# Performance work log

Hardware: AMD Instinct MI355X
Metric: run time of the kernel (lower is better)

The kernel has to match this reference:

```python
import jax, jax.numpy as jnp
import numpy as np

RADIUS = 5
KS = 2 * RADIUS + 1  # 11
SIGMA_X2 = 4.0 ** 2  # 16
SIGMA_I2 = 10.0 ** 2  # 100


def _patches(x):
    """x: [N,1,H,W] -> [N, H*W, KS, KS] zero-padded sliding windows (torch Unfold semantics)."""
    N, _, H, W = x.shape
    p = jax.lax.conv_general_dilated_patches(
        x, (KS, KS), (1, 1), [(RADIUS, RADIUS), (RADIUS, RADIUS)]
    )  # [N, KS*KS, H, W], channel dim ordered (kh, kw)
    return p.reshape(N, KS, KS, H * W).transpose(0, 3, 1, 2)


def _distance_map(dtype):
    d = (jnp.arange(KS, dtype=dtype) - RADIUS) ** 2
    return jnp.exp(-(d[:, None] + d[None, :]) / SIGMA_X2)  # [KS, KS]


def setup_inputs() -> dict:
    key = jax.random.key(0)
    k1, k2 = jax.random.split(key)
    images = jax.random.uniform(k1, (8, 1, 224, 224), dtype=jnp.float32)
    labels = jax.random.uniform(k2, (8, 4, 224, 224), dtype=jnp.float32)
    return {"images": images, "labels": labels}


def reference(images, labels):
    B, _, H, W = images.shape
    K = labels.shape[1]
    HW = H * W

    img = images * 255.0
    regions = _patches(img)                                   # [B,HW,KS,KS]
    mask = _patches(jnp.ones((1, 1, H, W), img.dtype))        # [1,HW,KS,KS], 0 on padding
    dist_map = _distance_map(img.dtype)                       # [KS,KS]

    i_f = img.reshape(B, HW)[:, :, None, None]                # center pixel intensity
    weights = dist_map * jnp.exp(-(regions - i_f) ** 2 / SIGMA_I2) * mask  # [B,HW,KS,KS]

    # class-prob patches for all classes at once
    P = _patches(labels.reshape(B * K, 1, H, W)).reshape(B, K, HW, KS, KS)

    num = jnp.einsum('bnij,bknij->bkn', weights, P)           # sum_j w_ij * p_j
    den = weights.sum(axis=(2, 3))                            # [B,HW], sum_j w_ij
    p_f = labels.reshape(B, K, HW)

    ratio = jnp.einsum('bkn,bkn->bk', p_f, num) / jnp.einsum('bkn,bn->bk', p_f, den)
    # per-class L1Loss(ratio, 0) = mean over batch of |ratio|; summed over classes
    ratio_sum = jnp.abs(ratio).mean(axis=0).sum()
    return K - ratio_sum
```

## Files before the change

kernel.cpp:

```cpp
#include <hip/hip_runtime.h>
#include <hip/hip_bf16.h>

typedef float f2 __attribute__((ext_vector_type(2)));
typedef float f4 __attribute__((ext_vector_type(4)));

constexpr int Hh = 224, Ww = 224, Bb = 8, Kc = 4, RAD = 5;

constexpr int TX = 32;
constexpr int TILEH = 16;
constexpr int SW = TX + 2 * RAD;
constexpr int SH = TILEH + 2 * RAD;
constexpr int SSTR = SW + 1;
constexpr int GXD = Ww / TX;
constexpr int GYD = Hh / TILEH;
constexpr int PB = GXD * GYD;

constexpr float LOG2E = 1.44269504f;
constexpr float KI = -0.01f * LOG2E;
constexpr float DSC = -0.0625f * LOG2E;
constexpr float D2[12] = {25.f,16.f,9.f,4.f,1.f,0.f,1.f,4.f,9.f,16.f,25.f,0.f};

static __device__ inline f4 splat4(float x) { return (f4){x, x, x, x}; }

__global__ __launch_bounds__(256, 3) void ncut_main(const float* __restrict__ images,
                                                    const float* __restrict__ labels,
                                                    float* __restrict__ acc) {
    __shared__ float simg[SH * SSTR];
    __shared__ f4    slab[SH * SSTR];
    __shared__ float red[4][8];

    const int b   = blockIdx.z;
    const int x0  = blockIdx.x * TX;
    const int y0  = blockIdx.y * TILEH;
    const int tid = threadIdx.x;

    const float* imgb = images + (size_t)b * (Hh * Ww);
    const float* labb = labels + (size_t)b * (Kc * Hh * Ww);

    for (int idx = tid; idx < SH * SSTR; idx += 256) {
        const int lx = idx % SSTR, ly = idx / SSTR;
        const int gx = x0 - RAD + lx, gy = y0 - RAD + ly;
        float iv = 1e19f;
        f4 lv = (f4){0.f, 0.f, 0.f, 0.f};
        if (lx < SW && gx >= 0 && gx < Ww && gy >= 0 && gy < Hh) {
            const int g = gy * Ww + gx;
            iv = imgb[g] * 255.0f;
            lv = (f4){labb[g], labb[Hh * Ww + g], labb[2 * Hh * Ww + g], labb[3 * Hh * Ww + g]};
        }
        simg[idx] = iv;
        slab[idx] = lv;
    }
    __syncthreads();

    const int tx = tid & 31;
    const int ty = tid >> 5;
    const int r0 = 2 * ty;

    const float c0 = simg[(r0 + RAD) * SSTR + tx + RAD];
    const float c1 = simg[(r0 + RAD + 1) * SSTR + tx + RAD];

    f4 num0 = splat4(0.f), num1 = splat4(0.f);
    f2 den0 = (f2){0.f, 0.f}, den1 = (f2){0.f, 0.f};

#pragma unroll
    for (int dr = 0; dr < 12; ++dr) {
        const int rowoff = (r0 + dr) * SSTR + tx;
#pragma unroll
        for (int i = 0; i < 6; ++i) {
            const f2 v  = (f2){simg[rowoff + 2 * i], simg[rowoff + 2 * i + 1]};
            const f4 p0 = slab[rowoff + 2 * i];
            const f4 p1 = slab[rowoff + 2 * i + 1];
            if (dr < 11) {
                const f2 base = (f2){(D2[2 * i] + D2[dr]) * DSC,
                                     (D2[2 * i + 1] + D2[dr]) * DSC};
                const f2 d = v - c0;
                const f2 a = __builtin_elementwise_fma(d * KI, d, base);
                const float e0 = __builtin_amdgcn_exp2f(a.x);
                const float e1 = __builtin_amdgcn_exp2f(a.y);
                den0 += (f2){e0, e1};
                num0 = __builtin_elementwise_fma(splat4(e0), p0, num0);
                num0 = __builtin_elementwise_fma(splat4(e1), p1, num0);
            }
            if (dr >= 1) {
                const f2 base = (f2){(D2[2 * i] + D2[dr - 1]) * DSC,
                                     (D2[2 * i + 1] + D2[dr - 1]) * DSC};
                const f2 d = v - c1;
                const f2 a = __builtin_elementwise_fma(d * KI, d, base);
                const float e0 = __builtin_amdgcn_exp2f(a.x);
                const float e1 = __builtin_amdgcn_exp2f(a.y);
                den1 += (f2){e0, e1};
                num1 = __builtin_elementwise_fma(splat4(e0), p0, num1);
                num1 = __builtin_elementwise_fma(splat4(e1), p1, num1);
            }
        }
    }

    const f4 pc0 = slab[(r0 + RAD) * SSTR + tx + RAD];
    const f4 pc1 = slab[(r0 + RAD + 1) * SSTR + tx + RAD];
    const float dn0 = den0.x + den0.y;
    const float dn1 = den1.x + den1.y;

    const f4 numv = pc0 * num0 + pc1 * num1;
    const f4 denv = pc0 * dn0 + pc1 * dn1;

    float vals[8] = {numv.x, numv.y, numv.z, numv.w, denv.x, denv.y, denv.z, denv.w};

#pragma unroll
    for (int i = 0; i < 8; ++i) {
        float v = vals[i];
#pragma unroll
        for (int off = 32; off > 0; off >>= 1) v += __shfl_down(v, off, 64);
        vals[i] = v;
    }

    const int wave = tid >> 6, lane = tid & 63;
    if (lane == 0) {
#pragma unroll
        for (int i = 0; i < 8; ++i) red[wave][i] = vals[i];
    }
    __syncthreads();

    if (tid < 8) {
        const int gid = blockIdx.x + GXD * blockIdx.y + GXD * GYD * blockIdx.z;
        acc[gid * 8 + tid] = red[0][tid] + red[1][tid] + red[2][tid] + red[3][tid];
    }
}

__global__ void ncut_final(const float* __restrict__ acc, float* __restrict__ out) {
    const int t = threadIdx.x;
    const int k = t & 3, b = (t >> 2) & 7, part = t >> 5;
    float s = 0.f;
    for (int j = 0; j < PB; ++j) s += acc[(b * PB + j) * 8 + k + 4 * part];
    const float den = __shfl(s, (t + 32) & 63, 64);
    float r = (t < 32) ? fabsf(s / den) : 0.f;
#pragma unroll
    for (int off = 32; off > 0; off >>= 1) r += __shfl_down(r, off, 64);
    if (t == 0) out[0] = (float)Kc - r * (1.0f / (float)Bb);
}

extern "C" void kernel_launch(void* const* d_in, const int* in_sizes, int n_in,
                              void* d_out, int out_size, void* d_ws, size_t ws_size,
                              hipStream_t stream) {
    const float* images = (const float*)d_in[0];
    const float* labels = (const float*)d_in[1];
    float* out = (float*)d_out;
    float* acc = (float*)d_ws;

    dim3 grid(GXD, GYD, Bb);
    ncut_main<<<grid, 256, 0, stream>>>(images, labels, acc);
    ncut_final<<<1, 64, 0, stream>>>(acc, out);
}
```

Measured before the change: 83.95 us.

## Compute four output rows per thread with 128-thread blocks and separable distance weights

Each thread now accumulates four vertically adjacent output pixels instead of two, so every shared-memory image and label load in a column window is reused across more centers. Blocks shrink to 128 threads. The spatial Gaussian is factored into an x term folded into the exponent and a per-row y weight that is multiplied after the exp. The row loop is no longer unrolled, and each weight costs an extra multiply. The loop also does some wasted work on out-of-band rows where the y weight is zero. Fewer threads per block and more registers per thread may reduce occupancy.

```diff
diff --git a/kernel.cpp b/kernel.cpp
--- a/kernel.cpp
+++ b/kernel.cpp
@@ -7,6 +7,7 @@
 constexpr int Hh = 224, Ww = 224, Bb = 8, Kc = 4, RAD = 5;
 
 constexpr int TX = 32;
+constexpr int T  = 4;
 constexpr int TILEH = 16;
 constexpr int SW = TX + 2 * RAD;
 constexpr int SH = TILEH + 2 * RAD;
@@ -16,18 +17,17 @@
 constexpr int PB = GXD * GYD;
 
 constexpr float LOG2E = 1.44269504f;
-constexpr float KI = -0.01f * LOG2E;
+constexpr float KI  = -0.01f * LOG2E;
 constexpr float DSC = -0.0625f * LOG2E;
-constexpr float D2[12] = {25.f,16.f,9.f,4.f,1.f,0.f,1.f,4.f,9.f,16.f,25.f,0.f};
 
 static __device__ inline f4 splat4(float x) { return (f4){x, x, x, x}; }
 
-__global__ __launch_bounds__(256, 3) void ncut_main(const float* __restrict__ images,
-                                                    const float* __restrict__ labels,
-                                                    float* __restrict__ acc) {
+__global__ __launch_bounds__(128) void ncut_main(const float* __restrict__ images,
+                                                 const float* __restrict__ labels,
+                                                 float* __restrict__ acc) {
     __shared__ float simg[SH * SSTR];
     __shared__ f4    slab[SH * SSTR];
-    __shared__ float red[4][8];
+    __shared__ float red[2][8];
 
     const int b   = blockIdx.z;
     const int x0  = blockIdx.x * TX;
@@ -37,7 +37,7 @@
     const float* imgb = images + (size_t)b * (Hh * Ww);
     const float* labb = labels + (size_t)b * (Kc * Hh * Ww);
 
-    for (int idx = tid; idx < SH * SSTR; idx += 256) {
+    for (int idx = tid; idx < SH * SSTR; idx += 128) {
         const int lx = idx % SSTR, ly = idx / SSTR;
         const int gx = x0 - RAD + lx, gy = y0 - RAD + ly;
         float iv = 1e19f;
@@ -52,56 +52,61 @@
     }
     __syncthreads();
 
-    const int tx = tid & 31;
-    const int ty = tid >> 5;
-    const int r0 = 2 * ty;
+    const int tx   = tid & 31;
+    const int trow = tid >> 5;
+    const int r0   = trow * T;
 
-    const float c0 = simg[(r0 + RAD) * SSTR + tx + RAD];
-    const float c1 = simg[(r0 + RAD + 1) * SSTR + tx + RAD];
+    float ci[T];
+#pragma unroll
+    for (int c = 0; c < T; ++c) ci[c] = simg[(r0 + c + RAD) * SSTR + tx + RAD];
 
-    f4 num0 = splat4(0.f), num1 = splat4(0.f);
-    f2 den0 = (f2){0.f, 0.f}, den1 = (f2){0.f, 0.f};
+    f4 num[T];
+    f2 den[T];
+#pragma unroll
+    for (int c = 0; c < T; ++c) { num[c] = splat4(0.f); den[c] = (f2){0.f, 0.f}; }
 
+    for (int dr = 0; dr < T + 10; ++dr) {
+        const int rowoff = (r0 + dr) * SSTR + tx;
+        float dyw[T];
 #pragma unroll
-    for (int dr = 0; dr < 12; ++dr) {
-        const int rowoff = (r0 + dr) * SSTR + tx;
+        for (int c = 0; c < T; ++c) {
+            const int   di = dr - c - RAD;
+            const float fd = (float)(di * di);
+            const float e  = __builtin_amdgcn_exp2f(fd * DSC);
+            dyw[c] = (fd <= 25.f) ? e : 0.f;
+        }
 #pragma unroll
         for (int i = 0; i < 6; ++i) {
             const f2 v  = (f2){simg[rowoff + 2 * i], simg[rowoff + 2 * i + 1]};
             const f4 p0 = slab[rowoff + 2 * i];
             const f4 p1 = slab[rowoff + 2 * i + 1];
-            if (dr < 11) {
-                const f2 base = (f2){(D2[2 * i] + D2[dr]) * DSC,
-                                     (D2[2 * i + 1] + D2[dr]) * DSC};
-                const f2 d = v - c0;
-                const f2 a = __builtin_elementwise_fma(d * KI, d, base);
-                const float e0 = __builtin_amdgcn_exp2f(a.x);
-                const float e1 = __builtin_amdgcn_exp2f(a.y);
-                den0 += (f2){e0, e1};
-                num0 = __builtin_elementwise_fma(splat4(e0), p0, num0);
-                num0 = __builtin_elementwise_fma(splat4(e1), p1, num0);
-            }
-            if (dr >= 1) {
-                const f2 base = (f2){(D2[2 * i] + D2[dr - 1]) * DSC,
-                                     (D2[2 * i + 1] + D2[dr - 1]) * DSC};
-                const f2 d = v - c1;
-                const f2 a = __builtin_elementwise_fma(d * KI, d, base);
-                const float e0 = __builtin_amdgcn_exp2f(a.x);
-                const float e1 = __builtin_amdgcn_exp2f(a.y);
-                den1 += (f2){e0, e1};
-                num1 = __builtin_elementwise_fma(splat4(e0), p0, num1);
-                num1 = __builtin_elementwise_fma(splat4(e1), p1, num1);
+            const float dxa = (float)((2 * i - 5) * (2 * i - 5)) * DSC;
+            const float dxb = (2 * i + 1 < 11)
+                                  ? (float)((2 * i - 4) * (2 * i - 4)) * DSC
+                                  : -1e38f;
+            const f2 dxt = (f2){dxa, dxb};
+#pragma unroll
+            for (int c = 0; c < T; ++c) {
+                const f2 d = v - ci[c];
+                f2 t = d * KI;
+                t = __builtin_elementwise_fma(t, d, dxt);
+                const float w0 = __builtin_amdgcn_exp2f(t.x) * dyw[c];
+                const float w1 = __builtin_amdgcn_exp2f(t.y) * dyw[c];
+                den[c] += (f2){w0, w1};
+                num[c] = __builtin_elementwise_fma(splat4(w0), p0, num[c]);
+                num[c] = __builtin_elementwise_fma(splat4(w1), p1, num[c]);
             }
         }
     }
 
-    const f4 pc0 = slab[(r0 + RAD) * SSTR + tx + RAD];
-    const f4 pc1 = slab[(r0 + RAD + 1) * SSTR + tx + RAD];
-    const float dn0 = den0.x + den0.y;
-    const float dn1 = den1.x + den1.y;
-
-    const f4 numv = pc0 * num0 + pc1 * num1;
-    const f4 denv = pc0 * dn0 + pc1 * dn1;
+    f4 numv = splat4(0.f);
+    f4 denv = splat4(0.f);
+#pragma unroll
+    for (int c = 0; c < T; ++c) {
+        const f4 pc = slab[(r0 + c + RAD) * SSTR + tx + RAD];
+        numv = __builtin_elementwise_fma(pc, num[c], numv);
+        denv = __builtin_elementwise_fma(pc, splat4(den[c].x + den[c].y), denv);
+    }
 
     float vals[8] = {numv.x, numv.y, numv.z, numv.w, denv.x, denv.y, denv.z, denv.w};
 
@@ -122,7 +127,7 @@
 
     if (tid < 8) {
         const int gid = blockIdx.x + GXD * blockIdx.y + GXD * GYD * blockIdx.z;
-        acc[gid * 8 + tid] = red[0][tid] + red[1][tid] + red[2][tid] + red[3][tid];
+        acc[gid * 8 + tid] = red[0][tid] + red[1][tid];
     }
 }
 
@@ -147,6 +152,6 @@
     float* acc = (float*)d_ws;
 
     dim3 grid(GXD, GYD, Bb);
-    ncut_main<<<grid, 256, 0, stream>>>(images, labels, acc);
+    ncut_main<<<grid, 128, 0, stream>>>(images, labels, acc);
     ncut_final<<<1, 64, 0, stream>>>(acc, out);
 }
```

Result: slower. 90.84 us (+8.2%).

## Halve tile height and split window rows across thread halves, factor dist weight

Applied to the files above, without the earlier changes.

Halves the tile height so each block covers 8 rows, and splits the 12 window rows of the 11x11 stencil between two halves of the 256 threads. This doubles the number of blocks and raises the occupancy target. The distance weight is factored into a per-row exp2 multiplier times a column term, which removes the branch on each row. The final reduction is spread across 256 threads with a shared-memory stage. In exchange, halo overhead per tile rises and each block loads more redundant shared memory.

```diff
diff --git a/kernel.cpp b/kernel.cpp
--- a/kernel.cpp
+++ b/kernel.cpp
@@ -7,7 +7,7 @@
 constexpr int Hh = 224, Ww = 224, Bb = 8, Kc = 4, RAD = 5;
 
 constexpr int TX = 32;
-constexpr int TILEH = 16;
+constexpr int TILEH = 8;
 constexpr int SW = TX + 2 * RAD;
 constexpr int SH = TILEH + 2 * RAD;
 constexpr int SSTR = SW + 1;
@@ -16,13 +16,12 @@
 constexpr int PB = GXD * GYD;
 
 constexpr float LOG2E = 1.44269504f;
-constexpr float KI = -0.01f * LOG2E;
+constexpr float KI  = -0.01f * LOG2E;
 constexpr float DSC = -0.0625f * LOG2E;
-constexpr float D2[12] = {25.f,16.f,9.f,4.f,1.f,0.f,1.f,4.f,9.f,16.f,25.f,0.f};
 
 static __device__ inline f4 splat4(float x) { return (f4){x, x, x, x}; }
 
-__global__ __launch_bounds__(256, 3) void ncut_main(const float* __restrict__ images,
+__global__ __launch_bounds__(256, 6) void ncut_main(const float* __restrict__ images,
                                                     const float* __restrict__ labels,
                                                     float* __restrict__ acc) {
     __shared__ float simg[SH * SSTR];
@@ -52,9 +51,10 @@
     }
     __syncthreads();
 
-    const int tx = tid & 31;
-    const int ty = tid >> 5;
-    const int r0 = 2 * ty;
+    const int tx   = tid & 31;
+    const int ty   = (tid >> 5) & 3;
+    const int half = tid >> 7;
+    const int r0   = 2 * ty;
 
     const float c0 = simg[(r0 + RAD) * SSTR + tx + RAD];
     const float c1 = simg[(r0 + RAD + 1) * SSTR + tx + RAD];
@@ -63,45 +63,46 @@
     f2 den0 = (f2){0.f, 0.f}, den1 = (f2){0.f, 0.f};
 
 #pragma unroll
-    for (int dr = 0; dr < 12; ++dr) {
+    for (int r = 0; r < 6; ++r) {
+        const int dr = half * 6 + r;
         const int rowoff = (r0 + dr) * SSTR + tx;
+        const int   di0 = dr - 5,        di1 = dr - 6;
+        const float fd0 = (float)(di0 * di0), fd1 = (float)(di1 * di1);
+        const float dyw0 = (fd0 <= 25.f) ? __builtin_amdgcn_exp2f(fd0 * DSC) : 0.f;
+        const float dyw1 = (fd1 <= 25.f) ? __builtin_amdgcn_exp2f(fd1 * DSC) : 0.f;
 #pragma unroll
         for (int i = 0; i < 6; ++i) {
             const f2 v  = (f2){simg[rowoff + 2 * i], simg[rowoff + 2 * i + 1]};
             const f4 p0 = slab[rowoff + 2 * i];
             const f4 p1 = slab[rowoff + 2 * i + 1];
-            if (dr < 11) {
-                const f2 base = (f2){(D2[2 * i] + D2[dr]) * DSC,
-                                     (D2[2 * i + 1] + D2[dr]) * DSC};
+            const f2 dxt = (f2){(float)((2 * i - 5) * (2 * i - 5)) * DSC,
+                                (float)((2 * i - 4) * (2 * i - 4)) * DSC};
+            {
                 const f2 d = v - c0;
-                const f2 a = __builtin_elementwise_fma(d * KI, d, base);
-                const float e0 = __builtin_amdgcn_exp2f(a.x);
-                const float e1 = __builtin_amdgcn_exp2f(a.y);
-                den0 += (f2){e0, e1};
-                num0 = __builtin_elementwise_fma(splat4(e0), p0, num0);
-                num0 = __builtin_elementwise_fma(splat4(e1), p1, num0);
+                const f2 t = __builtin_elementwise_fma(d * KI, d, dxt);
+                const float w0 = __builtin_amdgcn_exp2f(t.x) * dyw0;
+                const float w1 = __builtin_amdgcn_exp2f(t.y) * dyw0;
+                den0 += (f2){w0, w1};
+                num0 = __builtin_elementwise_fma(splat4(w0), p0, num0);
+                num0 = __builtin_elementwise_fma(splat4(w1), p1, num0);
             }
-            if (dr >= 1) {
-                const f2 base = (f2){(D2[2 * i] + D2[dr - 1]) * DSC,
-                                     (D2[2 * i + 1] + D2[dr - 1]) * DSC};
+            {
                 const f2 d = v - c1;
-                const f2 a = __builtin_elementwise_fma(d * KI, d, base);
-                const float e0 = __builtin_amdgcn_exp2f(a.x);
-                const float e1 = __builtin_amdgcn_exp2f(a.y);
-                den1 += (f2){e0, e1};
-                num1 = __builtin_elementwise_fma(splat4(e0), p0, num1);
-                num1 = __builtin_elementwise_fma(splat4(e1), p1, num1);
+                const f2 t = __builtin_elementwise_fma(d * KI, d, dxt);
+                const float w0 = __builtin_amdgcn_exp2f(t.x) * dyw1;
+                const float w1 = __builtin_amdgcn_exp2f(t.y) * dyw1;
+                den1 += (f2){w0, w1};
+                num1 = __builtin_elementwise_fma(splat4(w0), p0, num1);
+                num1 = __builtin_elementwise_fma(splat4(w1), p1, num1);
             }
         }
     }
 
     const f4 pc0 = slab[(r0 + RAD) * SSTR + tx + RAD];
     const f4 pc1 = slab[(r0 + RAD + 1) * SSTR + tx + RAD];
-    const float dn0 = den0.x + den0.y;
-    const float dn1 = den1.x + den1.y;
 
     const f4 numv = pc0 * num0 + pc1 * num1;
-    const f4 denv = pc0 * dn0 + pc1 * dn1;
+    const f4 denv = pc0 * (den0.x + den0.y) + pc1 * (den1.x + den1.y);
 
     float vals[8] = {numv.x, numv.y, numv.z, numv.w, denv.x, denv.y, denv.z, denv.w};
 
@@ -121,21 +122,34 @@
     __syncthreads();
 
     if (tid < 8) {
-        const int gid = blockIdx.x + GXD * blockIdx.y + GXD * GYD * blockIdx.z;
+        const int gid = blockIdx.x + GXD * blockIdx.y + PB * blockIdx.z;
         acc[gid * 8 + tid] = red[0][tid] + red[1][tid] + red[2][tid] + red[3][tid];
     }
 }
 
 __global__ void ncut_final(const float* __restrict__ acc, float* __restrict__ out) {
+    __shared__ float part[64];
     const int t = threadIdx.x;
-    const int k = t & 3, b = (t >> 2) & 7, part = t >> 5;
+    const int combo = t >> 2;
+    const int sub   = t & 3;
+    const int b   = combo >> 3;
+    const int idx = combo & 7;
     float s = 0.f;
-    for (int j = 0; j < PB; ++j) s += acc[(b * PB + j) * 8 + k + 4 * part];
-    const float den = __shfl(s, (t + 32) & 63, 64);
-    float r = (t < 32) ? fabsf(s / den) : 0.f;
+    for (int j = sub; j < PB; j += 4) s += acc[((size_t)(b * PB + j)) * 8 + idx];
+    s += __shfl_down(s, 2, 64);
+    s += __shfl_down(s, 1, 64);
+    if (sub == 0) part[combo] = s;
+    __syncthreads();
+    if (t < 64) {
+        float r = 0.f;
+        if (t < 32) {
+            const int bb = t >> 2, k = t & 3;
+            r = fabsf(part[(bb << 3) + k] / part[(bb << 3) + 4 + k]);
+        }
 #pragma unroll
-    for (int off = 32; off > 0; off >>= 1) r += __shfl_down(r, off, 64);
-    if (t == 0) out[0] = (float)Kc - r * (1.0f / (float)Bb);
+        for (int off = 32; off > 0; off >>= 1) r += __shfl_down(r, off, 64);
+        if (t == 0) out[0] = (float)Kc - r * (1.0f / (float)Bb);
+    }
 }
 
 extern "C" void kernel_launch(void* const* d_in, const int* in_sizes, int n_in,
@@ -148,5 +162,5 @@
 
     dim3 grid(GXD, GYD, Bb);
     ncut_main<<<grid, 256, 0, stream>>>(images, labels, acc);
-    ncut_final<<<1, 64, 0, stream>>>(acc, out);
+    ncut_final<<<1, 256, 0, stream>>>(acc, out);
 }
```

Measured after the change: 97.06 us. 1.16x slower.

## Halve tile height to double block count and parallelize final reduction

Applied to the files above, without the earlier changes.

Cuts the tile height from 16 to 8 rows and the block size from 256 to 128 threads, which doubles the number of blocks (1568 vs 784) so the grid fills the GPU's compute units better. The partial-sum buffer moves to a quantity-major layout so the final kernel can read it with coalesced accesses. The final kernel now uses 1024 threads with a shuffle-based tree reduction instead of 64 threads each looping serially over every block. Smaller tiles raise the share of redundant halo loads per output pixel.

```diff
diff --git a/kernel.cpp b/kernel.cpp
--- a/kernel.cpp
+++ b/kernel.cpp
@@ -7,27 +7,28 @@
 constexpr int Hh = 224, Ww = 224, Bb = 8, Kc = 4, RAD = 5;
 
 constexpr int TX = 32;
-constexpr int TILEH = 16;
+constexpr int TILEH = 8;
 constexpr int SW = TX + 2 * RAD;
 constexpr int SH = TILEH + 2 * RAD;
 constexpr int SSTR = SW + 1;
 constexpr int GXD = Ww / TX;
 constexpr int GYD = Hh / TILEH;
 constexpr int PB = GXD * GYD;
+constexpr int NB = PB * Bb;
 
 constexpr float LOG2E = 1.44269504f;
-constexpr float KI = -0.01f * LOG2E;
+constexpr float KI  = -0.01f * LOG2E;
 constexpr float DSC = -0.0625f * LOG2E;
 constexpr float D2[12] = {25.f,16.f,9.f,4.f,1.f,0.f,1.f,4.f,9.f,16.f,25.f,0.f};
 
 static __device__ inline f4 splat4(float x) { return (f4){x, x, x, x}; }
 
-__global__ __launch_bounds__(256, 3) void ncut_main(const float* __restrict__ images,
+__global__ __launch_bounds__(128, 3) void ncut_main(const float* __restrict__ images,
                                                     const float* __restrict__ labels,
                                                     float* __restrict__ acc) {
     __shared__ float simg[SH * SSTR];
     __shared__ f4    slab[SH * SSTR];
-    __shared__ float red[4][8];
+    __shared__ float red[2][8];
 
     const int b   = blockIdx.z;
     const int x0  = blockIdx.x * TX;
@@ -37,7 +38,7 @@
     const float* imgb = images + (size_t)b * (Hh * Ww);
     const float* labb = labels + (size_t)b * (Kc * Hh * Ww);
 
-    for (int idx = tid; idx < SH * SSTR; idx += 256) {
+    for (int idx = tid; idx < SH * SSTR; idx += 128) {
         const int lx = idx % SSTR, ly = idx / SSTR;
         const int gx = x0 - RAD + lx, gy = y0 - RAD + ly;
         float iv = 1e19f;
@@ -97,11 +98,9 @@
 
     const f4 pc0 = slab[(r0 + RAD) * SSTR + tx + RAD];
     const f4 pc1 = slab[(r0 + RAD + 1) * SSTR + tx + RAD];
-    const float dn0 = den0.x + den0.y;
-    const float dn1 = den1.x + den1.y;
 
     const f4 numv = pc0 * num0 + pc1 * num1;
-    const f4 denv = pc0 * dn0 + pc1 * dn1;
+    const f4 denv = pc0 * (den0.x + den0.y) + pc1 * (den1.x + den1.y);
 
     float vals[8] = {numv.x, numv.y, numv.z, numv.w, denv.x, denv.y, denv.z, denv.w};
 
@@ -121,21 +120,36 @@
     __syncthreads();
 
     if (tid < 8) {
-        const int gid = blockIdx.x + GXD * blockIdx.y + GXD * GYD * blockIdx.z;
-        acc[gid * 8 + tid] = red[0][tid] + red[1][tid] + red[2][tid] + red[3][tid];
+        const int gid = blockIdx.x + GXD * blockIdx.y + PB * blockIdx.z;
+        acc[tid * NB + gid] = red[0][tid] + red[1][tid];
     }
 }
 
 __global__ void ncut_final(const float* __restrict__ acc, float* __restrict__ out) {
+    __shared__ float part[64];
     const int t = threadIdx.x;
-    const int k = t & 3, b = (t >> 2) & 7, part = t >> 5;
+    const int combo = t >> 4;
+    const int sub   = t & 15;
+    const int idx = combo >> 3, b = combo & 7;
+    const float* p = acc + idx * NB + b * PB;
     float s = 0.f;
-    for (int j = 0; j < PB; ++j) s += acc[(b * PB + j) * 8 + k + 4 * part];
-    const float den = __shfl(s, (t + 32) & 63, 64);
-    float r = (t < 32) ? fabsf(s / den) : 0.f;
+    for (int j = sub; j < PB; j += 16) s += p[j];
+    s += __shfl_down(s, 8, 64);
+    s += __shfl_down(s, 4, 64);
+    s += __shfl_down(s, 2, 64);
+    s += __shfl_down(s, 1, 64);
+    if (sub == 0) part[combo] = s;
+    __syncthreads();
+    if (t < 64) {
+        float r = 0.f;
+        if (t < 32) {
+            const int k = t & 3, bb = t >> 2;
+            r = fabsf(part[k * 8 + bb] / part[(k + 4) * 8 + bb]);
+        }
 #pragma unroll
-    for (int off = 32; off > 0; off >>= 1) r += __shfl_down(r, off, 64);
-    if (t == 0) out[0] = (float)Kc - r * (1.0f / (float)Bb);
+        for (int off = 32; off > 0; off >>= 1) r += __shfl_down(r, off, 64);
+        if (t == 0) out[0] = (float)Kc - r * (1.0f / (float)Bb);
+    }
 }
 
 extern "C" void kernel_launch(void* const* d_in, const int* in_sizes, int n_in,
@@ -147,6 +161,6 @@
     float* acc = (float*)d_ws;
 
     dim3 grid(GXD, GYD, Bb);
-    ncut_main<<<grid, 256, 0, stream>>>(images, labels, acc);
-    ncut_final<<<1, 64, 0, stream>>>(acc, out);
+    ncut_main<<<grid, 128, 0, stream>>>(images, labels, acc);
+    ncut_final<<<1, 1024, 0, stream>>>(acc, out);
 }
```

New measurement: 85.60 us. Within noise of the previous version (+2.0%).
